# Performance work log

Hardware: AMD Instinct MI355X
Metric: run time of the kernel (lower is better)

## Reference

```python
import jax, jax.numpy as jnp
import numpy as np
from jax import lax

B, T, F, C = 2, 249, 64, 256   # fixed by alpha/beta weight shapes in build()
K = 3                          # conv kernel size
FILT = 256                     # q/k conv filters (both blocks)
V = 256                        # v conv filters (both blocks)
OUT_CH = 64                    # conv2d_final filters (hardcoded)


def conv2d(x, w, b):
    # NHWC 'same' conv, stride 1, dilation 1
    return lax.conv_general_dilated(
        x, w, window_strides=(1, 1), padding='SAME',
        dimension_numbers=('NHWC', 'HWIO', 'NHWC')) + b


def attn_block(x, wq, bq, wk, bk, wv, bv):
    # x: [B, H, L, C]; attention over L per (batch, H) slice
    q = conv2d(x, wq, bq)          # [B,H,L,FILT]
    k = conv2d(x, wk, bk)          # [B,H,L,FILT]
    v = conv2d(x, wv, bv)          # [B,H,L,V]
    scores = jnp.einsum('bhqc,bhkc->bhqk', q, k)   # [B,H,L,L]
    dist = jax.nn.softmax(scores, axis=-1)
    return jnp.einsum('bhqk,bhkc->bhqc', dist, v)  # [B,H,L,V]


def setup_inputs() -> dict:
    key = jax.random.key(0)
    ks = jax.random.split(key, 18)
    s = 0.05
    d = {'x': jax.random.normal(ks[0], (B, T, F, C), jnp.float32)}
    names = ['wq_f', 'wk_f', 'wv_f', 'wq_t', 'wk_t', 'wv_t']
    outs = [FILT, FILT, V, FILT, FILT, V]
    for i, (n, o) in enumerate(zip(names, outs)):
        d[n] = jax.random.normal(ks[1 + i], (K, K, C, o), jnp.float32) * s
        d['b' + n[1:]] = jnp.zeros((o,), jnp.float32)
    d['w_final'] = jax.random.normal(ks[8], (K, K, V + V + C, OUT_CH), jnp.float32) * s
    d['b_final'] = jnp.zeros((OUT_CH,), jnp.float32)
    d['alpha'] = jax.random.uniform(ks[9], (B, T, F, V), jnp.float32, -0.05, 0.05)
    d['beta'] = jax.random.uniform(ks[10], (B, T, F, V), jnp.float32, -0.05, 0.05)
    return d


def reference(x, wq_f, bq_f, wk_f, bk_f, wv_f, bv_f,
              wq_t, bq_t, wk_t, bk_t, wv_t, bv_t,
              w_final, b_final, alpha, beta):
    # AFAB: transpose to [B,F,T,C], attend over time axis T
    xt = jnp.transpose(x, (0, 2, 1, 3))
    out_freq = attn_block(xt, wq_f, bq_f, wk_f, bk_f, wv_f, bv_f)
    out_freq = jnp.transpose(out_freq, (0, 2, 1, 3))  # back to [B,T,F,V]
    # ATAB: attend over frequency axis F directly on [B,T,F,C]
    out_time = attn_block(x, wq_t, bq_t, wk_t, bk_t, wv_t, bv_t)
    # learned elementwise gating + concat + final conv (concatenation=True path)
    fused = jnp.concatenate([alpha * out_freq, beta * out_time, x], axis=-1)
    return conv2d(fused, w_final, b_final)
```

## Files before the change

kernel.cpp:

```cpp
#include <hip/hip_runtime.h>


typedef _Float16 f16;
typedef _Float16 f16x8 __attribute__((ext_vector_type(8)));
typedef float    f32x4 __attribute__((ext_vector_type(4)));

#define B_   2
#define T_   249
#define F_   64
#define TP   251
#define FP   66
#define PIXB (T_*F_)
#define NPIX (B_*PIXB)
#define LPAD 256

static constexpr size_t FUSED_BYTES = (size_t)B_*TP*FP*768*2;
static constexpr size_t XPAD_BYTES  = (size_t)B_*TP*FP*256*2;
static constexpr size_t QF_BYTES    = (size_t)B_*64*LPAD*256*2;
static constexpr size_t QT_BYTES    = (size_t)B_*T_*64*256*2;
static constexpr size_t WT_BYTES    = (size_t)9*1536*256*2;
static constexpr size_t WFT_BYTES   = (size_t)9*64*768*2;

static constexpr size_t OFF_FUSED = 0;
static constexpr size_t OFF_XPAD  = OFF_FUSED + FUSED_BYTES;
static constexpr size_t OFF_QF    = OFF_XPAD  + XPAD_BYTES;
static constexpr size_t OFF_KF    = OFF_QF + QF_BYTES;
static constexpr size_t OFF_VF    = OFF_KF + QF_BYTES;
static constexpr size_t OFF_QT    = OFF_VF + QF_BYTES;
static constexpr size_t OFF_KT    = OFF_QT + QT_BYTES;
static constexpr size_t OFF_VT    = OFF_KT + QT_BYTES;
static constexpr size_t OFF_WT    = OFF_VT + QT_BYTES;
static constexpr size_t OFF_WFT   = OFF_WT + WT_BYTES;
static constexpr size_t OFF_BALL  = OFF_WFT + WFT_BYTES;
static constexpr size_t OFF_BF    = OFF_BALL + 1536*4;
static constexpr size_t WS_NEED   = OFF_BF + 64*4;

__device__ __forceinline__ f32x4 mfma16(f16x8 a, f16x8 b, f32x4 c) {
    return __builtin_amdgcn_mfma_f32_16x16x32_f16(a, b, c, 0, 0, 0);
}

__device__ __forceinline__ void gl_lds16(const void* g, void* l) {
    __builtin_amdgcn_global_load_lds(
        (const __attribute__((address_space(1))) unsigned int*)(unsigned long long)g,
        (__attribute__((address_space(3))) unsigned int*)(unsigned int)(unsigned long long)l,
        16, 0, 0);
}

__global__ __launch_bounds__(256) void prep_w(
    const float* __restrict__ wqf, const float* __restrict__ wkf, const float* __restrict__ wvf,
    const float* __restrict__ wqt, const float* __restrict__ wkt, const float* __restrict__ wvt,
    const float* __restrict__ wfin,
    const float* __restrict__ bqf, const float* __restrict__ bkf, const float* __restrict__ bvf,
    const float* __restrict__ bqt, const float* __restrict__ bkt, const float* __restrict__ bvt,
    const float* __restrict__ bfin,
    f16* __restrict__ wT, f16* __restrict__ wfT,
    float* __restrict__ biasAll, float* __restrict__ biasF)
{
    int idx = blockIdx.x*256 + threadIdx.x;
    if (idx < 9*1536*256) {
        int tap = idx / (1536*256);
        int r   = idx - tap*(1536*256);
        int n = r >> 8, c = r & 255;
        int dt = tap/3 - 1, df = tap%3 - 1;
        int blk = n >> 8, nl = n & 255;
        const float* w; int kh, kw;
        if (blk < 3) { w = (blk==0) ? wqf : (blk==1) ? wkf : wvf; kh = df+1; kw = dt+1; }
        else         { w = (blk==3) ? wqt : (blk==4) ? wkt : wvt; kh = dt+1; kw = df+1; }
        wT[idx] = (f16)w[((kh*3 + kw)*256 + c)*256 + nl];
    }
    if (idx < 9*64*768) {
        int tap = idx / (64*768);
        int r   = idx - tap*(64*768);
        int oc = r / 768, cin = r - oc*768;
        int dt = tap/3 - 1, df = tap%3 - 1;
        wfT[idx] = (f16)wfin[(((dt+1)*3 + (df+1))*768 + cin)*64 + oc];
    }
    if (idx < 1536) {
        int blk = idx >> 8, nl = idx & 255;
        const float* bb = (blk==0)?bqf:(blk==1)?bkf:(blk==2)?bvf:(blk==3)?bqt:(blk==4)?bkt:bvt;
        biasAll[idx] = bb[nl];
    }
    if (idx < 64) biasF[idx] = bfin[idx];
}

__global__ __launch_bounds__(256) void prep_x(
    const float* __restrict__ x, f16* __restrict__ xpad, f16* __restrict__ fused)
{
    int tid = blockIdx.x*256 + threadIdx.x;
    int pix = tid >> 5, c8 = (tid & 31)*8;
    int b = pix / PIXB; int r = pix - b*PIXB;
    int t = r >> 6, f = r & 63;
    const float* src = x + (size_t)pix*256 + c8;
    f16x8 v;
#pragma unroll
    for (int j = 0; j < 8; ++j) v[j] = (f16)src[j];
    size_t pp = (size_t)(b*TP + t + 1)*FP + (f + 1);
    *(f16x8*)(xpad + pp*256 + c8) = v;
    *(f16x8*)(fused + pp*768 + 512 + c8) = v;
}

__global__ __launch_bounds__(256, 2) void conv_qkv(
    const f16* __restrict__ xpad, const f16* __restrict__ wT,
    const float* __restrict__ biasAll,
    f16* __restrict__ qf, f16* __restrict__ kf, f16* __restrict__ vf,
    f16* __restrict__ qt, f16* __restrict__ kt_, f16* __restrict__ vt)
{
    __shared__ f16 ldsA[128*64];
    __shared__ f16 ldsB[256*64];

    const int nwgq = 186, nwgr = 6;
    int xcd = blockIdx.x & 7, lin = blockIdx.x >> 3;
    int wg = (xcd < nwgr ? xcd*(nwgq+1) : nwgr*(nwgq+1) + (xcd-nwgr)*nwgq) + lin;
    const int mt = wg / 6;
    const int nt = wg - mt*6;

    const int l   = threadIdx.x & 63;
    const int wid = threadIdx.x >> 6;
    const int wm = wid >> 1, wn = wid & 1;

    int aSrc[4];
#pragma unroll
    for (int i = 0; i < 4; ++i) {
        int row = i*32 + wid*8 + (l >> 3);
        int ch  = (l & 7) ^ (row & 7);
        int p = mt*128 + row;
        int b = p / PIXB; int r = p - b*PIXB;
        int t = r >> 6, f = r & 63;
        aSrc[i] = ((b*TP + t + 1)*FP + (f + 1))*256 + ch*8;
    }
    int bSrc[8];
#pragma unroll
    for (int j = 0; j < 8; ++j) {
        int row = j*32 + wid*8 + (l >> 3);
        int ch  = (l & 7) ^ (row & 7);
        bSrc[j] = (nt*256 + row)*256 + ch*8;
    }

    int aRow[4], aSw[4], bRow[8], bSw[8];
#pragma unroll
    for (int mi = 0; mi < 4; ++mi) {
        int row = wm*64 + mi*16 + (l & 15);
        aRow[mi] = row*64; aSw[mi] = row & 7;
    }
#pragma unroll
    for (int ni = 0; ni < 8; ++ni) {
        int row = wn*128 + ni*16 + (l & 15);
        bRow[ni] = row*64; bSw[ni] = row & 7;
    }

    f32x4 acc[4][8];
#pragma unroll
    for (int mi = 0; mi < 4; ++mi)
#pragma unroll
        for (int ni = 0; ni < 8; ++ni) acc[mi][ni] = {0.f, 0.f, 0.f, 0.f};

    for (int tap = 0; tap < 9; ++tap) {
        const int dt = tap/3 - 1, df = tap%3 - 1;
        const int ash = (dt*FP + df)*256;
        const f16* wtap = wT + (size_t)tap*1536*256;
        for (int kc = 0; kc < 4; ++kc) {
            const int c0 = kc*64;
#pragma unroll
            for (int i = 0; i < 4; ++i)
                gl_lds16(xpad + aSrc[i] + ash + c0, ldsA + (i*32 + wid*8)*64);
#pragma unroll
            for (int j = 0; j < 8; ++j)
                gl_lds16(wtap + bSrc[j] + c0, ldsB + (j*32 + wid*8)*64);
            __syncthreads();
#pragma unroll
            for (int kk = 0; kk < 2; ++kk) {
                const int cch = kk*4 + (l >> 4);
                f16x8 af[4], bf[8];
#pragma unroll
                for (int mi = 0; mi < 4; ++mi)
                    af[mi] = *(const f16x8*)(ldsA + aRow[mi] + ((cch ^ aSw[mi]) << 3));
#pragma unroll
                for (int ni = 0; ni < 8; ++ni)
                    bf[ni] = *(const f16x8*)(ldsB + bRow[ni] + ((cch ^ bSw[ni]) << 3));
#pragma unroll
                for (int mi = 0; mi < 4; ++mi)
#pragma unroll
                    for (int ni = 0; ni < 8; ++ni)
                        acc[mi][ni] = mfma16(af[mi], bf[ni], acc[mi][ni]);
            }
            __syncthreads();
        }
    }

    f16* dst = (nt==0)?qf:(nt==1)?kf:(nt==2)?vf:(nt==3)?qt:(nt==4)?kt_:vt;
#pragma unroll
    for (int mi = 0; mi < 4; ++mi) {
#pragma unroll
        for (int rg = 0; rg < 4; ++rg) {
            int row = wm*64 + mi*16 + (l >> 4)*4 + rg;
            int p = mt*128 + row;
            int b = p / PIXB; int r = p - b*PIXB;
            int t = r >> 6, f = r & 63;
#pragma unroll
            for (int ni = 0; ni < 8; ++ni) {
                int col = wn*128 + ni*16 + (l & 15);
                float v = acc[mi][ni][rg] + biasAll[nt*256 + col];
                int off;
                if (nt < 2)       off = ((b*64 + f)*LPAD + t)*256 + col;
                else if (nt == 2) off = ((b*64 + f)*256 + col)*LPAD + t;
                else if (nt < 5)  off = ((b*T_ + t)*64 + f)*256 + col;
                else              off = ((b*T_ + t)*256 + col)*64 + f;
                dst[off] = (f16)v;
            }
        }
    }
}

__global__ __launch_bounds__(256) void attn_f(
    const f16* __restrict__ qf, const f16* __restrict__ kf, const f16* __restrict__ vf,
    const float* __restrict__ alpha, f16* __restrict__ fused)
{
    __shared__ f16 plds[4][16*256];
    const int l = threadIdx.x & 63;
    const int wid = threadIdx.x >> 6;
    const int head = blockIdx.x >> 2;
    const int qb = blockIdx.x & 3;
    const int b = head >> 6, f = head & 63;
    const f16* qh = qf + (size_t)head*LPAD*256;
    const f16* kh = kf + (size_t)head*LPAD*256;
    const f16* vh = vf + (size_t)head*256*LPAD;
    const int qr0 = qb*64 + wid*16;
    f16* pw = &plds[wid][0];

    f16x8 qa[8];
#pragma unroll
    for (int ks = 0; ks < 8; ++ks)
        qa[ks] = *(const f16x8*)(qh + (qr0 + (l & 15))*256 + ks*32 + (l >> 4)*8);

    f32x4 s[16];
#pragma unroll
    for (int nf = 0; nf < 16; ++nf) s[nf] = {0.f, 0.f, 0.f, 0.f};
#pragma unroll
    for (int ks = 0; ks < 8; ++ks)
#pragma unroll
        for (int nf = 0; nf < 16; ++nf) {
            f16x8 bf = *(const f16x8*)(kh + (nf*16 + (l & 15))*256 + ks*32 + (l >> 4)*8);
            s[nf] = mfma16(qa[ks], bf, s[nf]);
        }

    float inv[4];
#pragma unroll
    for (int rg = 0; rg < 4; ++rg) {
        float m = -1e30f;
#pragma unroll
        for (int nf = 0; nf < 16; ++nf)
            if (nf*16 + (l & 15) < T_) m = fmaxf(m, s[nf][rg]);
#pragma unroll
        for (int d = 1; d < 16; d <<= 1) m = fmaxf(m, __shfl_xor(m, d, 64));
        float sum = 0.f;
#pragma unroll
        for (int nf = 0; nf < 16; ++nf) {
            float p = (nf*16 + (l & 15) < T_) ? __expf(s[nf][rg] - m) : 0.f;
            s[nf][rg] = p;
            sum += p;
        }
#pragma unroll
        for (int d = 1; d < 16; d <<= 1) sum += __shfl_xor(sum, d, 64);
        inv[rg] = 1.f / sum;
    }

#pragma unroll
    for (int nf = 0; nf < 16; ++nf)
#pragma unroll
        for (int rg = 0; rg < 4; ++rg) {
            int row = (l >> 4)*4 + rg;
            int col = nf*16 + (l & 15);
            int byte = (row*512 + col*2) ^ ((row & 7) << 4);
            *(f16*)((char*)pw + byte) = (f16)s[nf][rg];
        }

    f32x4 o[16];
#pragma unroll
    for (int nf = 0; nf < 16; ++nf) o[nf] = {0.f, 0.f, 0.f, 0.f};
#pragma unroll
    for (int ks = 0; ks < 8; ++ks) {
        int row = l & 15;
        int cch = ks*4 + (l >> 4);
        int byte = row*512 + ((cch ^ (row & 7)) << 4);
        f16x8 pa = *(const f16x8*)((const char*)pw + byte);
#pragma unroll
        for (int nf = 0; nf < 16; ++nf) {
            f16x8 bf = *(const f16x8*)(vh + (nf*16 + (l & 15))*LPAD + ks*32 + (l >> 4)*8);
            o[nf] = mfma16(pa, bf, o[nf]);
        }
    }

#pragma unroll
    for (int rg = 0; rg < 4; ++rg) {
        int t = qr0 + (l >> 4)*4 + rg;
        if (t < T_) {
#pragma unroll
            for (int nf = 0; nf < 16; ++nf) {
                int c = nf*16 + (l & 15);
                float v = o[nf][rg] * inv[rg] * alpha[((size_t)(b*T_ + t)*64 + f)*256 + c];
                fused[((size_t)(b*TP + t + 1)*FP + (f + 1))*768 + c] = (f16)v;
            }
        }
    }
}

__global__ __launch_bounds__(256) void attn_t(
    const f16* __restrict__ qt, const f16* __restrict__ kt, const f16* __restrict__ vt,
    const float* __restrict__ beta, f16* __restrict__ fused)
{
    __shared__ f16 plds[4][16*64];
    const int l = threadIdx.x & 63;
    const int wid = threadIdx.x >> 6;
    const int head = blockIdx.x;
    const int b = head / T_, t = head - b*T_;
    const f16* qh = qt + (size_t)head*64*256;
    const f16* kh = kt + (size_t)head*64*256;
    const f16* vh = vt + (size_t)head*256*64;
    const int qr0 = wid*16;
    f16* pw = &plds[wid][0];

    f16x8 qa[8];
#pragma unroll
    for (int ks = 0; ks < 8; ++ks)
        qa[ks] = *(const f16x8*)(qh + (qr0 + (l & 15))*256 + ks*32 + (l >> 4)*8);

    f32x4 s[4];
#pragma unroll
    for (int nf = 0; nf < 4; ++nf) s[nf] = {0.f, 0.f, 0.f, 0.f};
#pragma unroll
    for (int ks = 0; ks < 8; ++ks)
#pragma unroll
        for (int nf = 0; nf < 4; ++nf) {
            f16x8 bf = *(const f16x8*)(kh + (nf*16 + (l & 15))*256 + ks*32 + (l >> 4)*8);
            s[nf] = mfma16(qa[ks], bf, s[nf]);
        }

    float inv[4];
#pragma unroll
    for (int rg = 0; rg < 4; ++rg) {
        float m = -1e30f;
#pragma unroll
        for (int nf = 0; nf < 4; ++nf) m = fmaxf(m, s[nf][rg]);
#pragma unroll
        for (int d = 1; d < 16; d <<= 1) m = fmaxf(m, __shfl_xor(m, d, 64));
        float sum = 0.f;
#pragma unroll
        for (int nf = 0; nf < 4; ++nf) {
            float p = __expf(s[nf][rg] - m);
            s[nf][rg] = p;
            sum += p;
        }
#pragma unroll
        for (int d = 1; d < 16; d <<= 1) sum += __shfl_xor(sum, d, 64);
        inv[rg] = 1.f / sum;
    }

#pragma unroll
    for (int nf = 0; nf < 4; ++nf)
#pragma unroll
        for (int rg = 0; rg < 4; ++rg) {
            int row = (l >> 4)*4 + rg;
            int col = nf*16 + (l & 15);
            int byte = (row*128 + col*2) ^ ((row & 7) << 4);
            *(f16*)((char*)pw + byte) = (f16)s[nf][rg];
        }

    f32x4 o[16];
#pragma unroll
    for (int nf = 0; nf < 16; ++nf) o[nf] = {0.f, 0.f, 0.f, 0.f};
#pragma unroll
    for (int ks = 0; ks < 2; ++ks) {
        int row = l & 15;
        int cch = ks*4 + (l >> 4);
        int byte = row*128 + ((cch ^ (row & 7)) << 4);
        f16x8 pa = *(const f16x8*)((const char*)pw + byte);
#pragma unroll
        for (int nf = 0; nf < 16; ++nf) {
            f16x8 bf = *(const f16x8*)(vh + (nf*16 + (l & 15))*64 + ks*32 + (l >> 4)*8);
            o[nf] = mfma16(pa, bf, o[nf]);
        }
    }

#pragma unroll
    for (int rg = 0; rg < 4; ++rg) {
        int fo = qr0 + (l >> 4)*4 + rg;
#pragma unroll
        for (int nf = 0; nf < 16; ++nf) {
            int c = nf*16 + (l & 15);
            float v = o[nf][rg] * inv[rg] * beta[((size_t)(b*T_ + t)*64 + fo)*256 + c];
            fused[((size_t)(b*TP + t + 1)*FP + (fo + 1))*768 + 256 + c] = (f16)v;
        }
    }
}

__global__ __launch_bounds__(256, 3) void conv_final(
    const f16* __restrict__ fused, const f16* __restrict__ wfT,
    const float* __restrict__ biasF, float* __restrict__ out)
{
    __shared__ f16 ldsA[64*128];
    __shared__ f16 ldsB[64*128];
    const int l = threadIdx.x & 63;
    const int wid = threadIdx.x >> 6;
    const int mt = blockIdx.x;
    const int b = mt / T_, t = mt - b*T_;

    int aSrc[4], bSrc[4];
#pragma unroll
    for (int i = 0; i < 4; ++i) {
        int row = i*16 + wid*4 + (l >> 4);
        int ch  = (l & 15) ^ (row & 7);
        aSrc[i] = ((b*TP + t + 1)*FP + (row + 1))*768 + ch*8;
        bSrc[i] = row*768 + ch*8;
    }

    int aRowOff, aSwz;
    {
        int row = wid*16 + (l & 15);
        aRowOff = row*128; aSwz = row & 7;
    }
    int bRow[4], bSw[4];
#pragma unroll
    for (int ni = 0; ni < 4; ++ni) {
        int row = ni*16 + (l & 15);
        bRow[ni] = row*128; bSw[ni] = row & 7;
    }

    f32x4 acc[4];
#pragma unroll
    for (int ni = 0; ni < 4; ++ni) acc[ni] = {0.f, 0.f, 0.f, 0.f};

    for (int tap = 0; tap < 9; ++tap) {
        const int dt = tap/3 - 1, df = tap%3 - 1;
        const int ash = (dt*FP + df)*768;
        const f16* wt = wfT + (size_t)tap*64*768;
        for (int kc = 0; kc < 6; ++kc) {
            const int c0 = kc*128;
#pragma unroll
            for (int i = 0; i < 4; ++i) {
                gl_lds16(fused + aSrc[i] + ash + c0, ldsA + (i*16 + wid*4)*128);
                gl_lds16(wt + bSrc[i] + c0,          ldsB + (i*16 + wid*4)*128);
            }
            __syncthreads();
#pragma unroll
            for (int kk = 0; kk < 4; ++kk) {
                const int cch = kk*4 + (l >> 4);
                f16x8 af = *(const f16x8*)(ldsA + aRowOff + ((cch ^ aSwz) << 3));
                f16x8 bf[4];
#pragma unroll
                for (int ni = 0; ni < 4; ++ni)
                    bf[ni] = *(const f16x8*)(ldsB + bRow[ni] + ((cch ^ bSw[ni]) << 3));
#pragma unroll
                for (int ni = 0; ni < 4; ++ni)
                    acc[ni] = mfma16(af, bf[ni], acc[ni]);
            }
            __syncthreads();
        }
    }

#pragma unroll
    for (int rg = 0; rg < 4; ++rg) {
        int f = wid*16 + (l >> 4)*4 + rg;
        int p = mt*64 + f;
#pragma unroll
        for (int ni = 0; ni < 4; ++ni) {
            int oc = ni*16 + (l & 15);
            out[(size_t)p*64 + oc] = acc[ni][rg] + biasF[oc];
        }
    }
}

extern "C" void kernel_launch(void* const* d_in, const int* in_sizes, int n_in,
                              void* d_out, int out_size, void* d_ws, size_t ws_size,
                              hipStream_t stream) {
    (void)in_sizes; (void)n_in; (void)out_size;
    const float* x    = (const float*)d_in[0];
    const float* wqf  = (const float*)d_in[1];
    const float* bqf  = (const float*)d_in[2];
    const float* wkf  = (const float*)d_in[3];
    const float* bkf  = (const float*)d_in[4];
    const float* wvf  = (const float*)d_in[5];
    const float* bvf  = (const float*)d_in[6];
    const float* wqt  = (const float*)d_in[7];
    const float* bqt  = (const float*)d_in[8];
    const float* wkt  = (const float*)d_in[9];
    const float* bkt  = (const float*)d_in[10];
    const float* wvt  = (const float*)d_in[11];
    const float* bvt  = (const float*)d_in[12];
    const float* wfin = (const float*)d_in[13];
    const float* bfin = (const float*)d_in[14];
    const float* alpha= (const float*)d_in[15];
    const float* beta = (const float*)d_in[16];

    if (ws_size < WS_NEED) return;

    char* ws = (char*)d_ws;
    f16* fused  = (f16*)(ws + OFF_FUSED);
    f16* xpad   = (f16*)(ws + OFF_XPAD);
    f16* qf     = (f16*)(ws + OFF_QF);
    f16* kf     = (f16*)(ws + OFF_KF);
    f16* vf     = (f16*)(ws + OFF_VF);
    f16* qt     = (f16*)(ws + OFF_QT);
    f16* kt     = (f16*)(ws + OFF_KT);
    f16* vt     = (f16*)(ws + OFF_VT);
    f16* wT     = (f16*)(ws + OFF_WT);
    f16* wfT    = (f16*)(ws + OFF_WFT);
    float* bAll = (float*)(ws + OFF_BALL);
    float* bF   = (float*)(ws + OFF_BF);

    hipMemsetAsync(fused, 0, FUSED_BYTES, stream);
    hipMemsetAsync(xpad,  0, XPAD_BYTES,  stream);
    hipMemsetAsync(vf,    0, QF_BYTES,    stream);

    prep_w<<<dim3((9*1536*256 + 255)/256), dim3(256), 0, stream>>>(
        wqf, wkf, wvf, wqt, wkt, wvt, wfin,
        bqf, bkf, bvf, bqt, bkt, bvt, bfin, wT, wfT, bAll, bF);
    prep_x<<<dim3(NPIX*32/256), dim3(256), 0, stream>>>(x, xpad, fused);
    conv_qkv<<<dim3(1494), dim3(256), 0, stream>>>(xpad, wT, bAll, qf, kf, vf, qt, kt, vt);
    attn_f<<<dim3(512), dim3(256), 0, stream>>>(qf, kf, vf, alpha, fused);
    attn_t<<<dim3(498), dim3(256), 0, stream>>>(qt, kt, vt, beta, fused);
    conv_final<<<dim3(498), dim3(256), 0, stream>>>(fused, wfT, bF, (float*)d_out);
}
```

Before: 587.2 us.

## Double-buffer LDS in conv kernels, shrink qkv N-tile, zero only padding borders

Both conv_qkv and conv_final now use two LDS stages, so the global-to-LDS load for the next K-chunk is issued while MFMAs run on the current one. MFMA blocks are also bracketed with s_setprio. conv_qkv's output tile drops from 128x256 to 128x128 and the grid doubles, which lowers accumulator pressure and adds waves, at the cost of reloading the A tile twice. The full memsets of the padded fused and xpad buffers are replaced by a small kernel that zeroes only the border pixels, cutting memset traffic.

```diff
diff --git a/kernel.cpp b/kernel.cpp
--- a/kernel.cpp
+++ b/kernel.cpp
@@ -99,95 +99,116 @@
     *(f16x8*)(fused + pp*768 + 512 + c8) = v;
 }
 
-__global__ __launch_bounds__(256, 2) void conv_qkv(
+__global__ __launch_bounds__(256) void border_zero(
+    f16* __restrict__ xpad, f16* __restrict__ fused)
+{
+    int pix = blockIdx.x*2 + (threadIdx.x >> 7);
+    int tl = threadIdx.x & 127;
+    int b = pix / 630; int i = pix - b*630;
+    int tp, fp;
+    if (i < 66)       { tp = 0;   fp = i; }
+    else if (i < 132) { tp = 250; fp = i - 66; }
+    else { int j = i - 132; tp = 1 + (j >> 1); fp = (j & 1) * 65; }
+    size_t pp = (size_t)(b*TP + tp)*FP + fp;
+    f16x8 z = {0, 0, 0, 0, 0, 0, 0, 0};
+    if (tl < 32) *(f16x8*)(xpad + pp*256 + tl*8) = z;
+    if (tl < 96) *(f16x8*)(fused + pp*768 + tl*8) = z;
+}
+
+__global__ __launch_bounds__(256) void conv_qkv(
     const f16* __restrict__ xpad, const f16* __restrict__ wT,
     const float* __restrict__ biasAll,
     f16* __restrict__ qf, f16* __restrict__ kf, f16* __restrict__ vf,
     f16* __restrict__ qt, f16* __restrict__ kt_, f16* __restrict__ vt)
 {
-    __shared__ f16 ldsA[128*64];
-    __shared__ f16 ldsB[256*64];
-
-    const int nwgq = 186, nwgr = 6;
+    __shared__ f16 smem[2][16384];
+    const int l   = threadIdx.x & 63;
+    const int wid = threadIdx.x >> 6;
+
+    const int nwgq = 373, nwgr = 4;
     int xcd = blockIdx.x & 7, lin = blockIdx.x >> 3;
     int wg = (xcd < nwgr ? xcd*(nwgq+1) : nwgr*(nwgq+1) + (xcd-nwgr)*nwgq) + lin;
-    const int mt = wg / 6;
-    const int nt = wg - mt*6;
-
-    const int l   = threadIdx.x & 63;
-    const int wid = threadIdx.x >> 6;
+    const int mt = wg / 12;
+    const int nt = wg - mt*12;
     const int wm = wid >> 1, wn = wid & 1;
 
-    int aSrc[4];
+    int aSrc[4], bSrc[4];
 #pragma unroll
     for (int i = 0; i < 4; ++i) {
-        int row = i*32 + wid*8 + (l >> 3);
+        int row = wid*32 + i*8 + (l >> 3);
         int ch  = (l & 7) ^ (row & 7);
         int p = mt*128 + row;
         int b = p / PIXB; int r = p - b*PIXB;
         int t = r >> 6, f = r & 63;
         aSrc[i] = ((b*TP + t + 1)*FP + (f + 1))*256 + ch*8;
-    }
-    int bSrc[8];
-#pragma unroll
-    for (int j = 0; j < 8; ++j) {
-        int row = j*32 + wid*8 + (l >> 3);
-        int ch  = (l & 7) ^ (row & 7);
-        bSrc[j] = (nt*256 + row)*256 + ch*8;
-    }
-
-    int aRow[4], aSw[4], bRow[8], bSw[8];
+        bSrc[i] = (nt*128 + row)*256 + ch*8;
+    }
+
+    int aRow[4], aSw[4], bRow[4], bSw[4];
 #pragma unroll
     for (int mi = 0; mi < 4; ++mi) {
         int row = wm*64 + mi*16 + (l & 15);
         aRow[mi] = row*64; aSw[mi] = row & 7;
     }
 #pragma unroll
-    for (int ni = 0; ni < 8; ++ni) {
-        int row = wn*128 + ni*16 + (l & 15);
-        bRow[ni] = row*64; bSw[ni] = row & 7;
-    }
-
-    f32x4 acc[4][8];
+    for (int ni = 0; ni < 4; ++ni) {
+        int row = wn*64 + ni*16 + (l & 15);
+        bRow[ni] = 8192 + row*64; bSw[ni] = row & 7;
+    }
+
+    f32x4 acc[4][4];
 #pragma unroll
     for (int mi = 0; mi < 4; ++mi)
 #pragma unroll
-        for (int ni = 0; ni < 8; ++ni) acc[mi][ni] = {0.f, 0.f, 0.f, 0.f};
-
-    for (int tap = 0; tap < 9; ++tap) {
-        const int dt = tap/3 - 1, df = tap%3 - 1;
-        const int ash = (dt*FP + df)*256;
-        const f16* wtap = wT + (size_t)tap*1536*256;
-        for (int kc = 0; kc < 4; ++kc) {
-            const int c0 = kc*64;
-#pragma unroll
-            for (int i = 0; i < 4; ++i)
-                gl_lds16(xpad + aSrc[i] + ash + c0, ldsA + (i*32 + wid*8)*64);
-#pragma unroll
-            for (int j = 0; j < 8; ++j)
-                gl_lds16(wtap + bSrc[j] + c0, ldsB + (j*32 + wid*8)*64);
-            __syncthreads();
-#pragma unroll
-            for (int kk = 0; kk < 2; ++kk) {
-                const int cch = kk*4 + (l >> 4);
-                f16x8 af[4], bf[8];
-#pragma unroll
-                for (int mi = 0; mi < 4; ++mi)
-                    af[mi] = *(const f16x8*)(ldsA + aRow[mi] + ((cch ^ aSw[mi]) << 3));
-#pragma unroll
-                for (int ni = 0; ni < 8; ++ni)
-                    bf[ni] = *(const f16x8*)(ldsB + bRow[ni] + ((cch ^ bSw[ni]) << 3));
-#pragma unroll
-                for (int mi = 0; mi < 4; ++mi)
-#pragma unroll
-                    for (int ni = 0; ni < 8; ++ni)
-                        acc[mi][ni] = mfma16(af[mi], bf[ni], acc[mi][ni]);
-            }
-            __syncthreads();
-        }
-    }
-
-    f16* dst = (nt==0)?qf:(nt==1)?kf:(nt==2)?vf:(nt==3)?qt:(nt==4)?kt_:vt;
+        for (int ni = 0; ni < 4; ++ni) acc[mi][ni] = {0.f, 0.f, 0.f, 0.f};
+
+#define QSTAGE(KN, NB) do {                                                    \
+        int tap_ = (KN) >> 2, kc_ = (KN) & 3;                                  \
+        int ash_ = ((tap_/3 - 1)*FP + (tap_%3 - 1))*256 + kc_*64;              \
+        const f16* wtap_ = wT + (size_t)tap_*(1536*256) + kc_*64;              \
+        _Pragma("unroll")                                                      \
+        for (int i_ = 0; i_ < 4; ++i_) {                                       \
+            gl_lds16(xpad + aSrc[i_] + ash_, &smem[NB][(wid*32 + i_*8)*64]);   \
+            gl_lds16(wtap_ + bSrc[i_], &smem[NB][8192 + (wid*32 + i_*8)*64]);  \
+        }                                                                      \
+    } while (0)
+
+#define QCOMP(NB) do {                                                         \
+        _Pragma("unroll")                                                      \
+        for (int kk = 0; kk < 2; ++kk) {                                       \
+            const int cch = kk*4 + (l >> 4);                                   \
+            f16x8 af[4], bf[4];                                                \
+            _Pragma("unroll")                                                  \
+            for (int mi = 0; mi < 4; ++mi)                                     \
+                af[mi] = *(const f16x8*)(&smem[NB][0] + aRow[mi] + ((cch ^ aSw[mi]) << 3)); \
+            _Pragma("unroll")                                                  \
+            for (int ni = 0; ni < 4; ++ni)                                     \
+                bf[ni] = *(const f16x8*)(&smem[NB][0] + bRow[ni] + ((cch ^ bSw[ni]) << 3)); \
+            __builtin_amdgcn_s_setprio(1);                                     \
+            _Pragma("unroll")                                                  \
+            for (int mi = 0; mi < 4; ++mi)                                     \
+                _Pragma("unroll")                                              \
+                for (int ni = 0; ni < 4; ++ni)                                 \
+                    acc[mi][ni] = mfma16(af[mi], bf[ni], acc[mi][ni]);         \
+            __builtin_amdgcn_s_setprio(0);                                     \
+        }                                                                      \
+    } while (0)
+
+    QSTAGE(0, 0);
+    __syncthreads();
+    for (int kn = 0; kn < 36; kn += 2) {
+        if (kn + 1 < 36) QSTAGE(kn + 1, 1);
+        QCOMP(0);
+        __syncthreads();
+        if (kn + 2 < 36) QSTAGE(kn + 2, 0);
+        QCOMP(1);
+        __syncthreads();
+    }
+#undef QSTAGE
+#undef QCOMP
+
+    const int buf = nt >> 1;
+    f16* dst = (buf==0)?qf:(buf==1)?kf:(buf==2)?vf:(buf==3)?qt:(buf==4)?kt_:vt;
 #pragma unroll
     for (int mi = 0; mi < 4; ++mi) {
 #pragma unroll
@@ -197,14 +218,16 @@
             int b = p / PIXB; int r = p - b*PIXB;
             int t = r >> 6, f = r & 63;
 #pragma unroll
-            for (int ni = 0; ni < 8; ++ni) {
-                int col = wn*128 + ni*16 + (l & 15);
-                float v = acc[mi][ni][rg] + biasAll[nt*256 + col];
+            for (int ni = 0; ni < 4; ++ni) {
+                int col = wn*64 + ni*16 + (l & 15);
+                int ocg = nt*128 + col;
+                int ocl = ocg & 255;
+                float v = acc[mi][ni][rg] + biasAll[ocg];
                 int off;
-                if (nt < 2)       off = ((b*64 + f)*LPAD + t)*256 + col;
-                else if (nt == 2) off = ((b*64 + f)*256 + col)*LPAD + t;
-                else if (nt < 5)  off = ((b*T_ + t)*64 + f)*256 + col;
-                else              off = ((b*T_ + t)*256 + col)*64 + f;
+                if (buf < 2)       off = ((b*64 + f)*LPAD + t)*256 + ocl;
+                else if (buf == 2) off = ((b*64 + f)*256 + ocl)*LPAD + t;
+                else if (buf < 5)  off = ((b*T_ + t)*64 + f)*256 + ocl;
+                else               off = ((b*T_ + t)*256 + ocl)*64 + f;
                 dst[off] = (f16)v;
             }
         }
@@ -393,12 +416,11 @@
     }
 }
 
-__global__ __launch_bounds__(256, 3) void conv_final(
+__global__ __launch_bounds__(256) void conv_final(
     const f16* __restrict__ fused, const f16* __restrict__ wfT,
     const float* __restrict__ biasF, float* __restrict__ out)
 {
-    __shared__ f16 ldsA[64*128];
-    __shared__ f16 ldsB[64*128];
+    __shared__ f16 smem[2][16384];
     const int l = threadIdx.x & 63;
     const int wid = threadIdx.x >> 6;
     const int mt = blockIdx.x;
@@ -414,48 +436,58 @@
     }
 
     int aRowOff, aSwz;
-    {
-        int row = wid*16 + (l & 15);
-        aRowOff = row*128; aSwz = row & 7;
-    }
+    { int row = wid*16 + (l & 15); aRowOff = row*128; aSwz = row & 7; }
     int bRow[4], bSw[4];
 #pragma unroll
     for (int ni = 0; ni < 4; ++ni) {
         int row = ni*16 + (l & 15);
-        bRow[ni] = row*128; bSw[ni] = row & 7;
+        bRow[ni] = 8192 + row*128; bSw[ni] = row & 7;
     }
 
     f32x4 acc[4];
 #pragma unroll
     for (int ni = 0; ni < 4; ++ni) acc[ni] = {0.f, 0.f, 0.f, 0.f};
 
-    for (int tap = 0; tap < 9; ++tap) {
-        const int dt = tap/3 - 1, df = tap%3 - 1;
-        const int ash = (dt*FP + df)*768;
-        const f16* wt = wfT + (size_t)tap*64*768;
-        for (int kc = 0; kc < 6; ++kc) {
-            const int c0 = kc*128;
-#pragma unroll
-            for (int i = 0; i < 4; ++i) {
-                gl_lds16(fused + aSrc[i] + ash + c0, ldsA + (i*16 + wid*4)*128);
-                gl_lds16(wt + bSrc[i] + c0,          ldsB + (i*16 + wid*4)*128);
-            }
-            __syncthreads();
-#pragma unroll
-            for (int kk = 0; kk < 4; ++kk) {
-                const int cch = kk*4 + (l >> 4);
-                f16x8 af = *(const f16x8*)(ldsA + aRowOff + ((cch ^ aSwz) << 3));
-                f16x8 bf[4];
-#pragma unroll
-                for (int ni = 0; ni < 4; ++ni)
-                    bf[ni] = *(const f16x8*)(ldsB + bRow[ni] + ((cch ^ bSw[ni]) << 3));
-#pragma unroll
-                for (int ni = 0; ni < 4; ++ni)
-                    acc[ni] = mfma16(af, bf[ni], acc[ni]);
-            }
-            __syncthreads();
-        }
-    }
+#define FSTAGE(KN, NB) do {                                                    \
+        int tap_ = (KN) / 6, kc_ = (KN) - ((KN)/6)*6;                          \
+        int ash_ = ((tap_/3 - 1)*FP + (tap_%3 - 1))*768 + kc_*128;             \
+        const f16* wt_ = wfT + (size_t)tap_*(64*768) + kc_*128;                \
+        _Pragma("unroll")                                                      \
+        for (int i_ = 0; i_ < 4; ++i_) {                                       \
+            gl_lds16(fused + aSrc[i_] + ash_, &smem[NB][(i_*16 + wid*4)*128]); \
+            gl_lds16(wt_ + bSrc[i_], &smem[NB][8192 + (i_*16 + wid*4)*128]);   \
+        }                                                                      \
+    } while (0)
+
+#define FCOMP(NB) do {                                                         \
+        _Pragma("unroll")                                                      \
+        for (int kk = 0; kk < 4; ++kk) {                                       \
+            const int cch = kk*4 + (l >> 4);                                   \
+            f16x8 af = *(const f16x8*)(&smem[NB][0] + aRowOff + ((cch ^ aSwz) << 3)); \
+            f16x8 bf[4];                                                       \
+            _Pragma("unroll")                                                  \
+            for (int ni = 0; ni < 4; ++ni)                                     \
+                bf[ni] = *(const f16x8*)(&smem[NB][0] + bRow[ni] + ((cch ^ bSw[ni]) << 3)); \
+            __builtin_amdgcn_s_setprio(1);                                     \
+            _Pragma("unroll")                                                  \
+            for (int ni = 0; ni < 4; ++ni)                                     \
+                acc[ni] = mfma16(af, bf[ni], acc[ni]);                         \
+            __builtin_amdgcn_s_setprio(0);                                     \
+        }                                                                      \
+    } while (0)
+
+    FSTAGE(0, 0);
+    __syncthreads();
+    for (int kn = 0; kn < 54; kn += 2) {
+        if (kn + 1 < 54) FSTAGE(kn + 1, 1);
+        FCOMP(0);
+        __syncthreads();
+        if (kn + 2 < 54) FSTAGE(kn + 2, 0);
+        FCOMP(1);
+        __syncthreads();
+    }
+#undef FSTAGE
+#undef FCOMP
 
 #pragma unroll
     for (int rg = 0; rg < 4; ++rg) {
@@ -507,15 +539,14 @@
     float* bAll = (float*)(ws + OFF_BALL);
     float* bF   = (float*)(ws + OFF_BF);
 
-    hipMemsetAsync(fused, 0, FUSED_BYTES, stream);
-    hipMemsetAsync(xpad,  0, XPAD_BYTES,  stream);
-    hipMemsetAsync(vf,    0, QF_BYTES,    stream);
-
+    hipMemsetAsync(vf, 0, QF_BYTES, stream);
+
+    border_zero<<<dim3(630), dim3(256), 0, stream>>>(xpad, fused);
     prep_w<<<dim3((9*1536*256 + 255)/256), dim3(256), 0, stream>>>(
         wqf, wkf, wvf, wqt, wkt, wvt, wfin,
         bqf, bkf, bvf, bqt, bkt, bvt, bfin, wT, wfT, bAll, bF);
     prep_x<<<dim3(NPIX*32/256), dim3(256), 0, stream>>>(x, xpad, fused);
-    conv_qkv<<<dim3(1494), dim3(256), 0, stream>>>(xpad, wT, bAll, qf, kf, vf, qt, kt, vt);
+    conv_qkv<<<dim3(2988), dim3(256), 0, stream>>>(xpad, wT, bAll, qf, kf, vf, qt, kt, vt);
     attn_f<<<dim3(512), dim3(256), 0, stream>>>(qf, kf, vf, alpha, fused);
     attn_t<<<dim3(498), dim3(256), 0, stream>>>(qt, kt, vt, beta, fused);
     conv_final<<<dim3(498), dim3(256), 0, stream>>>(fused, wfT, bF, (float*)d_out);
```

Result: faster. 509.5 us (-13.2%).
